# Performance work log

Measured on AMD Instinct MI355X. Metric: run time of the kernel, lower is better.

Reference implementation:

```python
import jax, jax.numpy as jnp
import numpy as np

VOCAB, N_EMBED, BLOCK = 32000, 256, 1024
B, T = 4, 1024

def setup_inputs() -> dict:
    key = jax.random.key(0)
    ks = jax.random.split(key, 9)
    s = 0.02
    return {
        "idx": jax.random.randint(ks[0], (B, T), 0, VOCAB),
        "targets": jax.random.randint(ks[1], (B, T), 0, VOCAB),
        "tok_table": jax.random.normal(ks[2], (VOCAB, N_EMBED), jnp.float32) * s,
        "pos_table": jax.random.normal(ks[3], (BLOCK, N_EMBED), jnp.float32) * s,
        "Wk": jax.random.normal(ks[4], (N_EMBED, N_EMBED), jnp.float32) * s,
        "Wq": jax.random.normal(ks[5], (N_EMBED, N_EMBED), jnp.float32) * s,
        "Wv": jax.random.normal(ks[6], (N_EMBED, N_EMBED), jnp.float32) * s,
        "lm_W": jax.random.normal(ks[7], (N_EMBED, VOCAB), jnp.float32) * s,
        "lm_b": jnp.zeros((VOCAB,), jnp.float32),
    }

def reference(idx, targets, tok_table, pos_table, Wk, Wq, Wv, lm_W, lm_b):
    Bv, Tv = idx.shape
    # embeddings
    x = tok_table[idx] + pos_table[:Tv]               # [B,T,E]
    C = x.shape[-1]
    # single causal self-attention head (head_size == n_embed)
    q = x @ Wq                                        # [B,T,E]
    k = x @ Wk
    v = x @ Wv
    wei = jnp.einsum('btc,bsc->bts', q, k) * (C ** -0.5)  # [B,T,T]
    causal = jnp.tril(jnp.ones((Tv, Tv), bool))
    wei = jnp.where(causal, wei, -jnp.inf)
    wei = jax.nn.softmax(wei, axis=-1)
    out = jnp.einsum('bts,bsc->btc', wei, v)          # [B,T,E]
    logits = out @ lm_W + lm_b                        # [B,T,V]
    logits_flat = logits.reshape(Bv * Tv, -1)
    tgt = targets.reshape(Bv * Tv)
    logp = jax.nn.log_softmax(logits_flat, axis=-1)
    loss = -jnp.mean(jnp.take_along_axis(logp, tgt[:, None], axis=1))
    return logits_flat, loss
```

## Files before the change

kernel.cpp:

```cpp
#include <hip/hip_runtime.h>
#include <hip/hip_bf16.h>
#include <math.h>

#define VOCAB 32000
#define EMB   256
#define TSEQ  1024
#define NROWS 4096

typedef __attribute__((ext_vector_type(8))) short short8;
typedef __attribute__((ext_vector_type(4))) float f32x4;

static __device__ __forceinline__ unsigned short bfb(float x) {
    __hip_bfloat16 h = __float2bfloat16(x);
    return *(unsigned short*)&h;
}
static __device__ __forceinline__ unsigned pk2(float a, float b) {
    return (unsigned)bfb(a) | ((unsigned)bfb(b) << 16);
}

__global__ __launch_bounds__(256) void k_pre(const float* __restrict__ lmW,
                                             const float* __restrict__ Wq,
                                             const float* __restrict__ Wk,
                                             const float* __restrict__ Wv,
                                             const int* __restrict__ idx,
                                             const float* __restrict__ tok,
                                             const float* __restrict__ pos,
                                             ushort* __restrict__ Wt,
                                             ushort* __restrict__ Wt3,
                                             ushort* __restrict__ xb) {
    int bx = blockIdx.x;
    if (bx >= 8192) {
        int row = bx - 8192;
        int t = row & (TSEQ - 1);
        int token = idx[row];
        int e = threadIdx.x;
        xb[row * EMB + e] = bfb(tok[token * EMB + e] + pos[t * EMB + e]);
        return;
    }
    __shared__ float T[32][33];
    const float* W; ushort* out; int n0, k0, ncols;
    if (bx < 8000) {
        W = lmW; out = Wt; n0 = (bx >> 3) * 32; k0 = (bx & 7) * 32; ncols = VOCAB;
    } else {
        int xi = bx - 8000;
        int z = xi >> 6, rem = xi & 63;
        W = (z == 0) ? Wq : (z == 1) ? Wk : Wv;
        out = Wt3 + (size_t)z * EMB * EMB;
        n0 = (rem >> 3) * 32; k0 = (rem & 7) * 32; ncols = EMB;
    }
    int tx = threadIdx.x & 31, ty = threadIdx.x >> 5;
    #pragma unroll
    for (int i = 0; i < 4; ++i) {
        int kk = ty + 8 * i;
        T[kk][tx] = W[(size_t)(k0 + kk) * ncols + n0 + tx];
    }
    __syncthreads();
    #pragma unroll
    for (int i = 0; i < 4; ++i) {
        int r = ty + 8 * i;
        out[(size_t)(n0 + r) * EMB + k0 + tx] = bfb(T[tx][r]);
    }
}

__global__ __launch_bounds__(256) void k_qkv_mm(const ushort* __restrict__ A,
                                                const ushort* __restrict__ Wt3,
                                                ushort* __restrict__ qb,
                                                ushort* __restrict__ kbf,
                                                ushort* __restrict__ vt) {
    __shared__ ushort As[128 * 64];
    __shared__ ushort Bs[128 * 64];

    int z = blockIdx.z;
    const ushort* Bt = Wt3 + (size_t)z * EMB * EMB;

    int m0 = blockIdx.x * 128, n0 = blockIdx.y * 128;
    int tid = threadIdx.x;
    int lane = tid & 63, wave = tid >> 6;
    int wm = wave >> 1, wn = wave & 1;
    int lr = lane >> 3, cc = lane & 7;
    int lrow = lane & 15, lk = lane >> 4;

    f32x4 acc[4][4];
    #pragma unroll
    for (int i = 0; i < 4; ++i)
        #pragma unroll
        for (int j = 0; j < 4; ++j)
            acc[i][j] = (f32x4){0.f, 0.f, 0.f, 0.f};

    for (int k0 = 0; k0 < EMB; k0 += 64) {
        #pragma unroll
        for (int j = 0; j < 4; ++j) {
            int rbase = j * 32 + wave * 8;
            int row = rbase + lr;
            int cs = cc ^ (row & 7);
            const ushort* ga = A + (size_t)(m0 + row) * EMB + k0 + cs * 8;
            const ushort* gb = Bt + (size_t)(n0 + row) * EMB + k0 + cs * 8;
            __builtin_amdgcn_global_load_lds(
                (const __attribute__((address_space(1))) void*)ga,
                (__attribute__((address_space(3))) void*)&As[rbase * 64], 16, 0, 0);
            __builtin_amdgcn_global_load_lds(
                (const __attribute__((address_space(1))) void*)gb,
                (__attribute__((address_space(3))) void*)&Bs[rbase * 64], 16, 0, 0);
        }
        __syncthreads();
        #pragma unroll
        for (int kk = 0; kk < 2; ++kk) {
            short8 a[4], b[4];
            #pragma unroll
            for (int m = 0; m < 4; ++m) {
                int row = wm * 64 + m * 16 + lrow;
                int c2 = (kk * 4 + lk) ^ (row & 7);
                a[m] = *(const short8*)&As[row * 64 + c2 * 8];
            }
            #pragma unroll
            for (int n = 0; n < 4; ++n) {
                int row = wn * 64 + n * 16 + lrow;
                int c2 = (kk * 4 + lk) ^ (row & 7);
                b[n] = *(const short8*)&Bs[row * 64 + c2 * 8];
            }
            if (z < 2) {
                #pragma unroll
                for (int m = 0; m < 4; ++m)
                    #pragma unroll
                    for (int n = 0; n < 4; ++n)
                        acc[m][n] = __builtin_amdgcn_mfma_f32_16x16x32_bf16(
                            b[n], a[m], acc[m][n], 0, 0, 0);
            } else {
                #pragma unroll
                for (int m = 0; m < 4; ++m)
                    #pragma unroll
                    for (int n = 0; n < 4; ++n)
                        acc[m][n] = __builtin_amdgcn_mfma_f32_16x16x32_bf16(
                            a[m], b[n], acc[m][n], 0, 0, 0);
            }
        }
        __syncthreads();
    }

    if (z < 2) {
        ushort* out = (z == 0) ? qb : kbf;
        #pragma unroll
        for (int m = 0; m < 4; ++m) {
            int token = m0 + wm * 64 + m * 16 + lrow;
            #pragma unroll
            for (int n = 0; n < 4; ++n) {
                uint2 w;
                w.x = pk2(acc[m][n][0], acc[m][n][1]);
                w.y = pk2(acc[m][n][2], acc[m][n][3]);
                *(uint2*)&out[(size_t)token * EMB + n0 + wn * 64 + n * 16 + lk * 4] = w;
            }
        }
    } else {
        #pragma unroll
        for (int n = 0; n < 4; ++n) {
            int e = n0 + wn * 64 + n * 16 + lrow;
            #pragma unroll
            for (int m = 0; m < 4; ++m) {
                int row = m0 + wm * 64 + m * 16 + lk * 4;
                int bb = row >> 10, rr = row & 1023;
                uint2 w;
                w.x = pk2(acc[m][n][0], acc[m][n][1]);
                w.y = pk2(acc[m][n][2], acc[m][n][3]);
                *(uint2*)&vt[((size_t)bb * EMB + e) * TSEQ + rr] = w;
            }
        }
    }
}

__global__ __launch_bounds__(512) void k_attn(const ushort* __restrict__ qg,
                                              const ushort* __restrict__ kg,
                                              const ushort* __restrict__ vt,
                                              ushort* __restrict__ ao) {
    __shared__ ushort K_s[2][32 * 256];
    __shared__ ushort V_s[2][256 * 32];

    int b = blockIdx.x >> 3;
    int g = blockIdx.x & 7;
    int wave = threadIdx.x >> 6;
    int lane = threadIdx.x & 63;
    int qbase = g * 128 + wave * 16;
    int q = lane & 15, lk = lane >> 4;

    const ushort* qrow = qg + (size_t)(b * TSEQ + qbase + q) * EMB;
    short8 qf[8];
    #pragma unroll
    for (int c = 0; c < 8; ++c)
        qf[c] = *(const short8*)&qrow[c * 32 + lk * 8];

    f32x4 o[16];
    #pragma unroll
    for (int i = 0; i < 16; ++i) o[i] = (f32x4){0.f, 0.f, 0.f, 0.f};
    float m_run = -1e30f, l_run = 0.f;

    auto STAGE = [&](int buf, int st) {
        const ushort* kbase = kg + (size_t)(b * TSEQ + st * 32) * EMB;
        #pragma unroll
        for (int i = 0; i < 2; ++i) {
            int t = wave * 2 + i;
            int r = t * 2 + (lane >> 5);
            int slot = lane & 31;
            int chunk = slot ^ (r & 7);
            const ushort* src = kbase + r * EMB + chunk * 8;
            __builtin_amdgcn_global_load_lds(
                (const __attribute__((address_space(1))) void*)src,
                (__attribute__((address_space(3))) void*)&K_s[buf][t * 512], 16, 0, 0);
        }
        #pragma unroll
        for (int i = 0; i < 2; ++i) {
            int t = wave * 2 + i;
            int e = t * 16 + (lane >> 2);
            int slot = lane & 3;
            int chunk = slot ^ (e & 3);
            const ushort* src = vt + ((size_t)b * EMB + e) * TSEQ + st * 32 + chunk * 8;
            __builtin_amdgcn_global_load_lds(
                (const __attribute__((address_space(1))) void*)src,
                (__attribute__((address_space(3))) void*)&V_s[buf][t * 512], 16, 0, 0);
        }
    };

    int wlast = (qbase + 15) >> 5;
    int glast = (g * 128 + 127) >> 5;
    STAGE(0, 0);
    int buf = 0;

    for (int st = 0; st <= glast; ++st) {
        if (st < glast) {
            STAGE(buf ^ 1, st + 1);
            asm volatile("s_waitcnt vmcnt(4)" ::: "memory");
        } else {
            asm volatile("s_waitcnt vmcnt(0)" ::: "memory");
        }
        __builtin_amdgcn_s_barrier();

        if (st <= wlast) {
            f32x4 sa0 = (f32x4){0.f, 0.f, 0.f, 0.f};
            f32x4 sa1 = (f32x4){0.f, 0.f, 0.f, 0.f};
            #pragma unroll
            for (int c = 0; c < 8; ++c) {
                int sl = (c * 4 + lk) ^ (q & 7);
                short8 kf0 = *(const short8*)&K_s[buf][q * 256 + sl * 8];
                short8 kf1 = *(const short8*)&K_s[buf][(16 + q) * 256 + sl * 8];
                sa0 = __builtin_amdgcn_mfma_f32_16x16x32_bf16(kf0, qf[c], sa0, 0, 0, 0);
                sa1 = __builtin_amdgcn_mfma_f32_16x16x32_bf16(kf1, qf[c], sa1, 0, 0, 0);
            }

            float sv0[4], sv1[4];
            #pragma unroll
            for (int j = 0; j < 4; ++j) { sv0[j] = sa0[j] * 0.0625f; sv1[j] = sa1[j] * 0.0625f; }
            if (st == wlast) {
                int qgl = qbase + q;
                #pragma unroll
                for (int j = 0; j < 4; ++j) {
                    if (st * 32 + lk * 4 + j > qgl)      sv0[j] = -1e30f;
                    if (st * 32 + 16 + lk * 4 + j > qgl) sv1[j] = -1e30f;
                }
            }

            float tm = sv0[0];
            #pragma unroll
            for (int j = 1; j < 4; ++j) tm = fmaxf(tm, sv0[j]);
            #pragma unroll
            for (int j = 0; j < 4; ++j) tm = fmaxf(tm, sv1[j]);
            tm = fmaxf(tm, __shfl_xor(tm, 16));
            tm = fmaxf(tm, __shfl_xor(tm, 32));
            float mn = fmaxf(m_run, tm);
            float alpha = __expf(m_run - mn);
            float p0[4], p1[4], ts = 0.f;
            #pragma unroll
            for (int j = 0; j < 4; ++j) {
                p0[j] = __expf(sv0[j] - mn);
                p1[j] = __expf(sv1[j] - mn);
                ts += p0[j] + p1[j];
            }
            ts += __shfl_xor(ts, 16);
            ts += __shfl_xor(ts, 32);
            l_run = l_run * alpha + ts;
            m_run = mn;

            #pragma unroll
            for (int i = 0; i < 16; ++i) {
                o[i][0] *= alpha; o[i][1] *= alpha; o[i][2] *= alpha; o[i][3] *= alpha;
            }

            unsigned c0 = pk2(p0[0], p0[1]), c1 = pk2(p0[2], p0[3]);
            unsigned d0 = pk2(p1[0], p1[1]), d1 = pk2(p1[2], p1[3]);
            int sA = q + 32 * (lk & 1);
            int sB = sA + 16;
            unsigned a0c = __shfl(c0, sA), a1c = __shfl(c1, sA);
            unsigned b0c = __shfl(c0, sB), b1c = __shfl(c1, sB);
            unsigned a0d = __shfl(d0, sA), a1d = __shfl(d1, sA);
            unsigned b0d = __shfl(d0, sB), b1d = __shfl(d1, sB);
            bool hi = (lk >> 1) != 0;
            union { short8 s; unsigned u[4]; } pb;
            pb.u[0] = hi ? a0d : a0c;
            pb.u[1] = hi ? a1d : a1c;
            pb.u[2] = hi ? b0d : b0c;
            pb.u[3] = hi ? b1d : b1c;

            #pragma unroll
            for (int eb = 0; eb < 16; ++eb) {
                int er = eb * 16 + q;
                int sl = lk ^ (er & 3);
                short8 vf = *(const short8*)&V_s[buf][er * 32 + sl * 8];
                o[eb] = __builtin_amdgcn_mfma_f32_16x16x32_bf16(vf, pb.s, o[eb], 0, 0, 0);
            }
        }
        __builtin_amdgcn_s_barrier();
        buf ^= 1;
    }

    float inv_l = 1.f / l_run;
    ushort* orow = ao + (size_t)(b * TSEQ + qbase + q) * EMB;
    #pragma unroll
    for (int eb = 0; eb < 16; ++eb) {
        uint2 w;
        w.x = pk2(o[eb][0] * inv_l, o[eb][1] * inv_l);
        w.y = pk2(o[eb][2] * inv_l, o[eb][3] * inv_l);
        *(uint2*)&orow[eb * 16 + lk * 4] = w;
    }
}

__global__ __launch_bounds__(256) void k_gemm(const ushort* __restrict__ A,
                                              const ushort* __restrict__ Bt,
                                              const float* __restrict__ lmb,
                                              float* __restrict__ C,
                                              float* __restrict__ rowsum) {
    __shared__ ushort As[2][128 * 64];
    __shared__ ushort Bs[2][128 * 64];

    int linear = blockIdx.x;
    int swz = (linear & 7) * 1000 + (linear >> 3);
    int m0 = (swz & 31) * 128;
    int nb = swz >> 5;
    int n0 = nb * 128;

    int tid = threadIdx.x;
    int lane = tid & 63, wave = tid >> 6;
    int wm = wave >> 1, wn = wave & 1;
    int lr = lane >> 3, cc = lane & 7;
    int lrow = lane & 15, lk = lane >> 4;

    auto STAGE = [&](int bufi, int k0) {
        #pragma unroll
        for (int j = 0; j < 4; ++j) {
            int rbase = j * 32 + wave * 8;
            int row = rbase + lr;
            int cs = cc ^ (row & 7);
            const ushort* ga = A + (size_t)(m0 + row) * EMB + k0 + cs * 8;
            const ushort* gb = Bt + (size_t)(n0 + row) * EMB + k0 + cs * 8;
            __builtin_amdgcn_global_load_lds(
                (const __attribute__((address_space(1))) void*)ga,
                (__attribute__((address_space(3))) void*)&As[bufi][rbase * 64], 16, 0, 0);
            __builtin_amdgcn_global_load_lds(
                (const __attribute__((address_space(1))) void*)gb,
                (__attribute__((address_space(3))) void*)&Bs[bufi][rbase * 64], 16, 0, 0);
        }
    };

    f32x4 acc[4][4];
    #pragma unroll
    for (int i = 0; i < 4; ++i)
        #pragma unroll
        for (int j = 0; j < 4; ++j)
            acc[i][j] = (f32x4){0.f, 0.f, 0.f, 0.f};

    STAGE(0, 0);
    asm volatile("s_waitcnt vmcnt(0)" ::: "memory");
    __syncthreads();

    #pragma unroll
    for (int t = 0; t < 4; ++t) {
        if (t < 3) STAGE((t + 1) & 1, (t + 1) * 64);
        const ushort* Ab = As[t & 1];
        const ushort* Bb = Bs[t & 1];
        #pragma unroll
        for (int kk = 0; kk < 2; ++kk) {
            short8 a[4], b[4];
            #pragma unroll
            for (int m = 0; m < 4; ++m) {
                int row = wm * 64 + m * 16 + lrow;
                int c2 = (kk * 4 + lk) ^ (row & 7);
                a[m] = *(const short8*)&Ab[row * 64 + c2 * 8];
            }
            #pragma unroll
            for (int n = 0; n < 4; ++n) {
                int row = wn * 64 + n * 16 + lrow;
                int c2 = (kk * 4 + lk) ^ (row & 7);
                b[n] = *(const short8*)&Bb[row * 64 + c2 * 8];
            }
            #pragma unroll
            for (int m = 0; m < 4; ++m)
                #pragma unroll
                for (int n = 0; n < 4; ++n)
                    acc[m][n] = __builtin_amdgcn_mfma_f32_16x16x32_bf16(
                        b[n], a[m], acc[m][n], 0, 0, 0);
        }
        if (t < 3) {
            asm volatile("s_waitcnt vmcnt(0)" ::: "memory");
            __syncthreads();
        }
    }

    f32x4 bias4[4];
    #pragma unroll
    for (int n = 0; n < 4; ++n)
        bias4[n] = *(const f32x4*)&lmb[n0 + wn * 64 + n * 16 + lk * 4];

    #pragma unroll
    for (int m = 0; m < 4; ++m) {
        int token = m0 + wm * 64 + m * 16 + lrow;
        #pragma unroll
        for (int n = 0; n < 4; ++n) {
            f32x4 v = acc[m][n] + bias4[n];
            __builtin_nontemporal_store(v,
                (f32x4*)&C[(size_t)token * VOCAB + n0 + wn * 64 + n * 16 + lk * 4]);
        }
    }

    #pragma unroll
    for (int m = 0; m < 4; ++m) {
        float tS = 0.f;
        #pragma unroll
        for (int n = 0; n < 4; ++n)
            #pragma unroll
            for (int j = 0; j < 4; ++j)
                tS += __expf(acc[m][n][j] + bias4[n][j]);
        tS += __shfl_xor(tS, 16);
        tS += __shfl_xor(tS, 32);
        if (lk == 0)
            atomicAdd(&rowsum[m0 + wm * 64 + m * 16 + lrow], tS);
    }
}

__global__ __launch_bounds__(256) void k_loss(const float* __restrict__ rowsum,
                                              const float* __restrict__ logits,
                                              const int* __restrict__ tgt,
                                              float* __restrict__ loss) {
    int row = blockIdx.x * 256 + threadIdx.x;
    float lse = __logf(rowsum[row]);
    float tl = logits[(size_t)row * VOCAB + tgt[row]];
    float c = (lse - tl) * (1.0f / 4096.0f);
    #pragma unroll
    for (int off = 1; off < 64; off <<= 1)
        c += __shfl_xor(c, off);
    __shared__ float ws4[4];
    int lane = threadIdx.x & 63, wave = threadIdx.x >> 6;
    if (lane == 0) ws4[wave] = c;
    __syncthreads();
    if (threadIdx.x == 0)
        atomicAdd(loss, ws4[0] + ws4[1] + ws4[2] + ws4[3]);
}

extern "C" void kernel_launch(void* const* d_in, const int* in_sizes, int n_in,
                              void* d_out, int out_size, void* d_ws, size_t ws_size,
                              hipStream_t stream) {
    (void)in_sizes; (void)n_in; (void)ws_size;
    const int*   idx     = (const int*)d_in[0];
    const int*   targets = (const int*)d_in[1];
    const float* tok     = (const float*)d_in[2];
    const float* pos     = (const float*)d_in[3];
    const float* Wk      = (const float*)d_in[4];
    const float* Wq      = (const float*)d_in[5];
    const float* Wv      = (const float*)d_in[6];
    const float* lmW     = (const float*)d_in[7];
    const float* lmb     = (const float*)d_in[8];

    float* logits = (float*)d_out;
    float* loss   = logits + (size_t)out_size - 1;

    const size_t MB = 1u << 20;
    char* w = (char*)d_ws;
    ushort* Wt3   = (ushort*)(w);
    float*  rowsum = (float*)(w + 448 * 1024);
    ushort* xb    = (ushort*)(w + MB / 2);
    ushort* qb    = (ushort*)(w + 5 * MB / 2);
    ushort* kbf   = (ushort*)(w + 9 * MB / 2);
    ushort* vt    = (ushort*)(w + 13 * MB / 2);
    ushort* ao    = (ushort*)(w + 17 * MB / 2);
    ushort* Wt    = (ushort*)(w + 21 * MB / 2);

    hipMemsetAsync(loss, 0, sizeof(float), stream);
    hipMemsetAsync(rowsum, 0, NROWS * sizeof(float), stream);
    k_pre<<<12288, 256, 0, stream>>>(lmW, Wq, Wk, Wv, idx, tok, pos, Wt, Wt3, xb);
    k_qkv_mm<<<dim3(NROWS / 128, EMB / 128, 3), 256, 0, stream>>>(xb, Wt3, qb, kbf, vt);
    k_attn<<<32, 512, 0, stream>>>(qb, kbf, vt, ao);
    k_gemm<<<8000, 256, 0, stream>>>(ao, Wt, lmb, logits, rowsum);
    k_loss<<<NROWS / 256, 256, 0, stream>>>(rowsum, logits, targets, loss);
}
```

Measured before the change: 277.5 us.

## Overlap lm_W transpose-to-bf16 with attention kernel using spare blocks

Moves the 32000x256 lm_W transpose and bf16 conversion out of the preprocessing kernel and into extra blocks appended to the attention launch. Attention uses only 32 blocks and leaves most CUs idle, so the conversion blocks can fill them and run concurrently. This shortens the critical path before the QKV matmul. The cost is that conversion blocks reuse attention's large shared-memory allocation, which may limit occupancy, and block scheduling order could delay the attention blocks.

```diff
diff --git a/kernel.cpp b/kernel.cpp
--- a/kernel.cpp
+++ b/kernel.cpp
@@ -18,19 +18,17 @@
     return (unsigned)bfb(a) | ((unsigned)bfb(b) << 16);
 }
 
-__global__ __launch_bounds__(256) void k_pre(const float* __restrict__ lmW,
-                                             const float* __restrict__ Wq,
+__global__ __launch_bounds__(256) void k_pre(const float* __restrict__ Wq,
                                              const float* __restrict__ Wk,
                                              const float* __restrict__ Wv,
                                              const int* __restrict__ idx,
                                              const float* __restrict__ tok,
                                              const float* __restrict__ pos,
-                                             ushort* __restrict__ Wt,
                                              ushort* __restrict__ Wt3,
                                              ushort* __restrict__ xb) {
     int bx = blockIdx.x;
-    if (bx >= 8192) {
-        int row = bx - 8192;
+    if (bx >= 192) {
+        int row = bx - 192;
         int t = row & (TSEQ - 1);
         int token = idx[row];
         int e = threadIdx.x;
@@ -38,21 +36,15 @@
         return;
     }
     __shared__ float T[32][33];
-    const float* W; ushort* out; int n0, k0, ncols;
-    if (bx < 8000) {
-        W = lmW; out = Wt; n0 = (bx >> 3) * 32; k0 = (bx & 7) * 32; ncols = VOCAB;
-    } else {
-        int xi = bx - 8000;
-        int z = xi >> 6, rem = xi & 63;
-        W = (z == 0) ? Wq : (z == 1) ? Wk : Wv;
-        out = Wt3 + (size_t)z * EMB * EMB;
-        n0 = (rem >> 3) * 32; k0 = (rem & 7) * 32; ncols = EMB;
-    }
+    int z = bx >> 6, rem = bx & 63;
+    const float* W = (z == 0) ? Wq : (z == 1) ? Wk : Wv;
+    ushort* out = Wt3 + (size_t)z * EMB * EMB;
+    int n0 = (rem >> 3) * 32, k0 = (rem & 7) * 32;
     int tx = threadIdx.x & 31, ty = threadIdx.x >> 5;
     #pragma unroll
     for (int i = 0; i < 4; ++i) {
         int kk = ty + 8 * i;
-        T[kk][tx] = W[(size_t)(k0 + kk) * ncols + n0 + tx];
+        T[kk][tx] = W[(size_t)(k0 + kk) * EMB + n0 + tx];
     }
     __syncthreads();
     #pragma unroll
@@ -167,12 +159,35 @@
     }
 }
 
-__global__ __launch_bounds__(512) void k_attn(const ushort* __restrict__ qg,
-                                              const ushort* __restrict__ kg,
-                                              const ushort* __restrict__ vt,
-                                              ushort* __restrict__ ao) {
+__global__ __launch_bounds__(512) void k_attn_conv(const ushort* __restrict__ qg,
+                                                   const ushort* __restrict__ kg,
+                                                   const ushort* __restrict__ vt,
+                                                   ushort* __restrict__ ao,
+                                                   const float* __restrict__ lmW,
+                                                   ushort* __restrict__ Wt) {
     __shared__ ushort K_s[2][32 * 256];
     __shared__ ushort V_s[2][256 * 32];
+
+    if (blockIdx.x >= 32) {
+        int t = threadIdx.x & 255;
+        int half = threadIdx.x >> 8;
+        int tile = (blockIdx.x - 32) * 2 + half;
+        int n0 = (tile >> 3) * 32, k0 = (tile & 7) * 32;
+        float* T = (float*)&K_s[0][0] + half * (32 * 33);
+        int tx = t & 31, ty = t >> 5;
+        #pragma unroll
+        for (int i = 0; i < 4; ++i) {
+            int kk = ty + 8 * i;
+            T[kk * 33 + tx] = lmW[(size_t)(k0 + kk) * VOCAB + n0 + tx];
+        }
+        __syncthreads();
+        #pragma unroll
+        for (int i = 0; i < 4; ++i) {
+            int r = ty + 8 * i;
+            Wt[(size_t)(n0 + r) * EMB + k0 + tx] = bfb(T[tx * 33 + r]);
+        }
+        return;
+    }
 
     int b = blockIdx.x >> 3;
     int g = blockIdx.x & 7;
@@ -481,9 +496,9 @@
 
     hipMemsetAsync(loss, 0, sizeof(float), stream);
     hipMemsetAsync(rowsum, 0, NROWS * sizeof(float), stream);
-    k_pre<<<12288, 256, 0, stream>>>(lmW, Wq, Wk, Wv, idx, tok, pos, Wt, Wt3, xb);
+    k_pre<<<4288, 256, 0, stream>>>(Wq, Wk, Wv, idx, tok, pos, Wt3, xb);
     k_qkv_mm<<<dim3(NROWS / 128, EMB / 128, 3), 256, 0, stream>>>(xb, Wt3, qb, kbf, vt);
-    k_attn<<<32, 512, 0, stream>>>(qb, kbf, vt, ao);
+    k_attn_conv<<<4032, 512, 0, stream>>>(qb, kbf, vt, ao, lmW, Wt);
     k_gemm<<<8000, 256, 0, stream>>>(ao, Wt, lmb, logits, rowsum);
     k_loss<<<NROWS / 256, 256, 0, stream>>>(rowsum, logits, targets, loss);
 }
```

After: 270.0 us. 1.03x faster.
